# Kernel optimization log

Hardware: AMD Instinct MI355X
Metric: run time of the kernel (lower is better)

Reference implementation:

```python
import jax, jax.numpy as jnp
import numpy as np

OBS_DIM = 115
ID_LO, ID_HI = 97, 108  # one-hot agent-id slice


def setup_inputs() -> dict:
    key = jax.random.key(0)
    k1, k2 = jax.random.split(key)
    a, b, n_agents = 128, 512, 11
    state_dim = n_agents * OBS_DIM  # 1265
    agents_q = jax.random.normal(k1, (a, b, n_agents), dtype=jnp.float32)
    global_state = jax.random.normal(k2, (a, b, state_dim), dtype=jnp.float32)
    return {"agents_q": agents_q, "global_state": global_state}


def reference(agents_q, global_state):
    a, b, n_agents = agents_q.shape
    q = agents_q.reshape(-1, n_agents)                 # [B, A]
    gs = global_state.reshape(-1, global_state.shape[-1])  # [B, A*115]
    B = q.shape[0]

    ball_pos = gs[:, 88:90]                            # [B, 2]
    holder_info = gs[:, 94:97]
    is_my_team = holder_info[:, 1] != 0                # .bool() semantics
    goal = jnp.array([1.0, 0.0], dtype=q.dtype)
    ball_goal_dist = jnp.sqrt(jnp.sum((ball_pos - goal) ** 2, axis=1))
    valid_advance = is_my_team & (ball_goal_dist > 0.19) & (ball_goal_dist < 0.99)

    # all agent obs blocks at once: [B, A, 115]
    obs = gs[:, : n_agents * OBS_DIM].reshape(B, n_agents, OBS_DIM)
    agent_id = jnp.argmax(obs[:, :, ID_LO:ID_HI], axis=-1)        # [B, A] in [0,10]
    pos_x = jnp.take_along_axis(obs, (2 * agent_id)[..., None], axis=-1)[..., 0]
    pos_y = jnp.take_along_axis(obs, (2 * agent_id + 1)[..., None], axis=-1)[..., 0]

    # distance of each agent to ball and to goal: [B, A]
    dist_matrix = jnp.sqrt((pos_x - ball_pos[:, 0:1]) ** 2 + (pos_y - ball_pos[:, 1:2]) ** 2)
    goal_dist_matrix = jnp.sqrt((pos_x - 1.0) ** 2 + pos_y ** 2)

    holder_mask = jax.nn.one_hot(jnp.argmin(dist_matrix, axis=1), n_agents, dtype=q.dtype)
    advance_component = holder_mask * valid_advance[:, None].astype(q.dtype) * 5.0
    position_component = 1.0 / (goal_dist_matrix + 1e-6)
    combined = jnp.where(valid_advance[:, None], advance_component, position_component)

    weights = jax.nn.softmax(combined, axis=1)
    global_q = jnp.sum(q * weights, axis=1, keepdims=True)        # [B, 1]
    return (global_q * n_agents).reshape(a, b, 1)
```

## Files before the change

kernel.cpp:

```cpp
#include <hip/hip_runtime.h>
#include <math.h>

#define OBS_DIM 115
#define N_AGENTS 11
#define TPR 16
#define ROWS_PER_BLOCK 16

__global__ __launch_bounds__(256) void qmix_kernel(
    const float* __restrict__ q,
    const float* __restrict__ gs,
    float* __restrict__ out,
    int B)
{
    const int tid = threadIdx.x;
    const int g   = tid >> 4;
    const int s   = tid & 15;
    const int r   = blockIdx.x * ROWS_PER_BLOCK + g;
    if (r >= B) return;

    const float* row = gs + (size_t)r * (N_AGENTS * OBS_DIM);

    float bx = row[88];
    float by = row[89];
    float team = row[95];
    float g0 = bx - 1.0f;
    float bgd = sqrtf(g0 * g0 + by * by);
    bool valid = (team != 0.0f) && (bgd > 0.19f) && (bgd < 0.99f);

    float dist = INFINITY;
    float comb = -INFINITY;
    float qv = 0.0f;
    float gd = 0.0f;

    if (s < N_AGENTS) {
        const float* base = row + s * OBS_DIM;
        float best = base[97];
        int bi = 0;
        #pragma unroll
        for (int j = 1; j < 11; ++j) {
            float v = base[97 + j];
            if (v > best) { best = v; bi = j; }
        }
        float px = base[2 * bi];
        float py = base[2 * bi + 1];
        float dx = px - bx, dy = py - by;
        dist = sqrtf(dx * dx + dy * dy);
        float gx = px - 1.0f;
        gd = sqrtf(gx * gx + py * py);
        qv = q[(size_t)r * N_AGENTS + s];
    }

    int idx = s;
    float d = dist;
    #pragma unroll
    for (int off = 8; off >= 1; off >>= 1) {
        float d2 = __shfl_xor(d, off, TPR);
        int   i2 = __shfl_xor(idx, off, TPR);
        if (d2 < d || (d2 == d && i2 < idx)) { d = d2; idx = i2; }
    }

    if (s < N_AGENTS) {
        comb = valid ? ((s == idx) ? 5.0f : 0.0f)
                     : 1.0f / (gd + 1e-6f);
    }

    float m = comb;
    #pragma unroll
    for (int off = 8; off >= 1; off >>= 1)
        m = fmaxf(m, __shfl_xor(m, off, TPR));

    float w  = expf(comb - m);
    float wq = w * qv;
    #pragma unroll
    for (int off = 8; off >= 1; off >>= 1) {
        w  += __shfl_xor(w,  off, TPR);
        wq += __shfl_xor(wq, off, TPR);
    }

    if (s == 0)
        out[r] = wq * (float)N_AGENTS / w;
}

extern "C" void kernel_launch(void* const* d_in, const int* in_sizes, int n_in,
                              void* d_out, int out_size, void* d_ws, size_t ws_size,
                              hipStream_t stream) {
    const float* q  = (const float*)d_in[0];
    const float* gs = (const float*)d_in[1];
    float* out = (float*)d_out;

    int B = in_sizes[0] / N_AGENTS;
    int grid = (B + ROWS_PER_BLOCK - 1) / ROWS_PER_BLOCK;
    qmix_kernel<<<grid, 256, 0, stream>>>(q, gs, out, B);
}
```

Before: 399.7 us.

## Gather needed row fields into LDS via global_load_lds before compute

```diff
diff --git a/kernel.cpp b/kernel.cpp
--- a/kernel.cpp
+++ b/kernel.cpp
@@ -3,8 +3,16 @@
 
 #define OBS_DIM 115
 #define N_AGENTS 11
-#define TPR 16
-#define ROWS_PER_BLOCK 16
+#define ROW_F (N_AGENTS * OBS_DIM)
+#define WAVES_PER_BLOCK 4
+#define ROWS_PER_WAVE 4
+#define ROWS_PER_BLOCK (WAVES_PER_BLOCK * ROWS_PER_WAVE)
+#define SLICE_F 388
+#define WAVE_F (ROWS_PER_WAVE * SLICE_F)
+
+
+typedef const __attribute__((address_space(1))) unsigned int gu32;
+typedef __attribute__((address_space(3))) unsigned int lu32;
 
 __global__ __launch_bounds__(256) void qmix_kernel(
     const float* __restrict__ q,
@@ -12,73 +20,105 @@
     float* __restrict__ out,
     int B)
 {
-    const int tid = threadIdx.x;
-    const int g   = tid >> 4;
-    const int s   = tid & 15;
-    const int r   = blockIdx.x * ROWS_PER_BLOCK + g;
-    if (r >= B) return;
+    __shared__ float lds[WAVES_PER_BLOCK * WAVE_F];
 
-    const float* row = gs + (size_t)r * (N_AGENTS * OBS_DIM);
+    const int tid  = threadIdx.x;
+    const int wv   = tid >> 6;
+    const int lane = tid & 63;
+    const int rbase = blockIdx.x * ROWS_PER_BLOCK + wv * ROWS_PER_WAVE;
 
-    float bx = row[88];
-    float by = row[89];
-    float team = row[95];
-    float g0 = bx - 1.0f;
-    float bgd = sqrtf(g0 * g0 + by * by);
-    bool valid = (team != 0.0f) && (bgd > 0.19f) && (bgd < 0.99f);
+    int off[6], isq[6];
+    #pragma unroll
+    for (int p6 = 0; p6 < 6; ++p6) {
+        const int mm = p6 * 64 + lane;
+        int o = 0, iq = 0;
+        if (mm < 242)      { const int a = mm / 22; o = a * OBS_DIM + (mm - a * 22); }
+        else if (mm < 363) { const int t = mm - 242; const int a = t / 11;
+                             o = a * OBS_DIM + 97 + (t - a * 11); }
+        else if (mm == 363) o = 88;
+        else if (mm == 364) o = 89;
+        else if (mm == 365) o = 95;
+        else if (mm < 377) { o = mm - 366; iq = 1; }
+        else               o = 0;
+        off[p6] = o; isq[p6] = iq;
+    }
+
+    #pragma unroll
+    for (int p = 0; p < ROWS_PER_WAVE * 6; ++p) {
+        const int rl = p / 6;
+        const int p6 = p % 6;
+        int rr = rbase + rl;
+        if (rr >= B) rr = B - 1;
+        const float* gbase = isq[p6] ? (q + (size_t)rr * N_AGENTS)
+                                     : (gs + (size_t)rr * ROW_F);
+        const float* src = gbase + off[p6];
+        __builtin_amdgcn_global_load_lds(
+            (gu32*)src,
+            (lu32*)&lds[wv * WAVE_F + rl * SLICE_F + p6 * 64],
+            4, 0, 0);
+    }
+
+    __syncthreads();
+
+    const int g  = lane >> 4;
+    const int s  = lane & 15;
+    const int rr = rbase + g;
+    const float* S = &lds[wv * WAVE_F + g * SLICE_F];
+
+    const float bx = S[363], by = S[364], team = S[365];
+    const float g0  = bx - 1.0f;
+    const float bgd = sqrtf(g0 * g0 + by * by);
+    const bool valid = (team != 0.0f) && (bgd > 0.19f) && (bgd < 0.99f);
 
     float dist = INFINITY;
     float comb = -INFINITY;
-    float qv = 0.0f;
-    float gd = 0.0f;
+    float qv = 0.0f, gd = 0.0f;
 
     if (s < N_AGENTS) {
-        const float* base = row + s * OBS_DIM;
-        float best = base[97];
-        int bi = 0;
+        const float* idb = S + 242 + s * 11;
+        float best = idb[0]; int bi = 0;
         #pragma unroll
         for (int j = 1; j < 11; ++j) {
-            float v = base[97 + j];
+            float v = idb[j];
             if (v > best) { best = v; bi = j; }
         }
-        float px = base[2 * bi];
-        float py = base[2 * bi + 1];
-        float dx = px - bx, dy = py - by;
+        const float px = S[s * 22 + 2 * bi];
+        const float py = S[s * 22 + 2 * bi + 1];
+        const float dx = px - bx, dy = py - by;
         dist = sqrtf(dx * dx + dy * dy);
-        float gx = px - 1.0f;
+        const float gx = px - 1.0f;
         gd = sqrtf(gx * gx + py * py);
-        qv = q[(size_t)r * N_AGENTS + s];
+        qv = S[366 + s];
     }
 
     int idx = s;
     float d = dist;
     #pragma unroll
-    for (int off = 8; off >= 1; off >>= 1) {
-        float d2 = __shfl_xor(d, off, TPR);
-        int   i2 = __shfl_xor(idx, off, TPR);
+    for (int o = 8; o >= 1; o >>= 1) {
+        float d2 = __shfl_xor(d, o, 16);
+        int   i2 = __shfl_xor(idx, o, 16);
         if (d2 < d || (d2 == d && i2 < idx)) { d = d2; idx = i2; }
     }
 
-    if (s < N_AGENTS) {
+    if (s < N_AGENTS)
         comb = valid ? ((s == idx) ? 5.0f : 0.0f)
                      : 1.0f / (gd + 1e-6f);
-    }
 
     float m = comb;
     #pragma unroll
-    for (int off = 8; off >= 1; off >>= 1)
-        m = fmaxf(m, __shfl_xor(m, off, TPR));
+    for (int o = 8; o >= 1; o >>= 1)
+        m = fmaxf(m, __shfl_xor(m, o, 16));
 
-    float w  = expf(comb - m);
-    float wq = w * qv;
+    float wgt = expf(comb - m);
+    float wq  = wgt * qv;
     #pragma unroll
-    for (int off = 8; off >= 1; off >>= 1) {
-        w  += __shfl_xor(w,  off, TPR);
-        wq += __shfl_xor(wq, off, TPR);
+    for (int o = 8; o >= 1; o >>= 1) {
+        wgt += __shfl_xor(wgt, o, 16);
+        wq  += __shfl_xor(wq,  o, 16);
     }
 
-    if (s == 0)
-        out[r] = wq * (float)N_AGENTS / w;
+    if (s == 0 && rr < B)
+        out[rr] = wq * (float)N_AGENTS / wgt;
 }
 
 extern "C" void kernel_launch(void* const* d_in, const int* in_sizes, int n_in,
```

Measured after the change: 409.5 us. 1.02x slower.
